# Optimization experiments

Measured on AMD Instinct MI355X. Metric: run time of the kernel, lower is better.

The kernel has to match this reference:

```python
import jax, jax.numpy as jnp
import numpy as np

CP_DIMS = (8, 8)      # control-point grid (matches init cp_dims)
EPS = 1e-10           # epsilon used by tf interpolate_spline _phi


def ndgrid(dims):
    """Normalized (y, x) grid, shape [prod(dims), 2], values in [0, 1]."""
    g = np.mgrid[:dims[0], :dims[1]].reshape(2, -1).T.astype(np.float32)
    g = g / (np.array(dims, dtype=np.float32) - 1.0)
    return jnp.asarray(g)


def _phi(r2):
    # order-2 TPS kernel on SQUARED distances: 0.5 * r2 * log(max(r2, eps))
    return 0.5 * r2 * jnp.log(jnp.maximum(r2, EPS))


def _sq_dist(a, b):
    # a: [m, d], b: [n, d] -> [m, n] squared distances
    d = a[:, None, :] - b[None, :, :]
    return jnp.sum(d * d, axis=-1)


def setup_inputs() -> dict:
    key = jax.random.key(0)
    k1, k2 = jax.random.split(key)
    vol = jax.random.normal(k1, (16, 256, 256, 16), dtype=jnp.float32)
    # small offsets in normalized [0,1] coordinates
    cp_offsets = jax.random.normal(k2, (16, 64, 2), dtype=jnp.float32) * 0.05
    return {"vol": vol, "cp_offsets": cp_offsets}


def reference(vol, cp_offsets):
    B, H, W, C = vol.shape
    cp = ndgrid(CP_DIMS)          # [n, 2] train points (fixed, inverse=False)
    q = ndgrid((H, W))            # [m, 2] query points
    n = cp.shape[0]
    m = q.shape[0]

    # ---- TPS solve (train points fixed across batch -> single LHS) ----
    A = _phi(_sq_dist(cp, cp))                              # [n, n]
    Bmat = jnp.concatenate([cp, jnp.ones((n, 1), cp.dtype)], axis=1)  # [n, 3]
    top = jnp.concatenate([A, Bmat], axis=1)                # [n, n+3]
    bot = jnp.concatenate([Bmat.T, jnp.zeros((3, 3), cp.dtype)], axis=1)
    lhs = jnp.concatenate([top, bot], axis=0)               # [n+3, n+3]

    warped = cp[None, :, :] + cp_offsets                    # [B, n, 2] train values
    rhs = jnp.concatenate([warped, jnp.zeros((B, 3, 2), vol.dtype)], axis=1)
    wv = jnp.linalg.solve(lhs[None], rhs)                   # [B, n+3, 2]
    w, v = wv[:, :n, :], wv[:, n:, :]                       # [B,n,2], [B,3,2]

    # ---- TPS apply at all pixel locations ----
    phi_q = _phi(_sq_dist(q, cp))                           # [m, n]
    q_aug = jnp.concatenate([q, jnp.ones((m, 1), q.dtype)], axis=1)  # [m, 3]
    loc = jnp.einsum('mn,bnk->bmk', phi_q, w) + jnp.einsum('mp,bpk->bmk', q_aug, v)
    # loc is (y, x) normalized; reverse -> (x, y) then scale to pixels
    x = loc[..., 1] * (W - 1)                               # [B, m]
    y = loc[..., 0] * (H - 1)

    # ---- bilinear resampling with zero padding (tf resampler semantics) ----
    x0 = jnp.floor(x); y0 = jnp.floor(y)
    wx = x - x0; wy = y - y0
    x0i = x0.astype(jnp.int32); y0i = y0.astype(jnp.int32)
    x1i = x0i + 1; y1i = y0i + 1

    vol_flat = vol.reshape(B, H * W, C)

    def gather(yi, xi):
        valid = (yi >= 0) & (yi < H) & (xi >= 0) & (xi < W)
        idx = jnp.clip(yi, 0, H - 1) * W + jnp.clip(xi, 0, W - 1)  # [B, m]
        vals = jnp.take_along_axis(vol_flat, idx[..., None], axis=1)  # [B, m, C]
        return vals * valid[..., None].astype(vol.dtype)

    out = (gather(y0i, x0i) * ((1 - wy) * (1 - wx))[..., None]
           + gather(y0i, x1i) * ((1 - wy) * wx)[..., None]
           + gather(y1i, x0i) * (wy * (1 - wx))[..., None]
           + gather(y1i, x1i) * (wy * wx)[..., None])
    return out.reshape(B, H, W, C)
```

## Files before the change

### kernel.cpp

```cpp
#include <hip/hip_runtime.h>
#include <math.h>
#include <string.h>

#define HH 256
#define WW 256
#define CC 16
#define BB 16
#define NCP 64
#define NA 67
#define WVS 68

typedef float f32x4 __attribute__((ext_vector_type(4)));

static void build_M(float* Mf , float* wv0 )
{
    static double A[NA][NA + NCP];
    for (int r = 0; r < NA; ++r) {
        for (int c = 0; c < NA; ++c) {
            double val;
            if (r < NCP && c < NCP) {
                double ry = (double)(r >> 3) / 7.0, rx = (double)(r & 7) / 7.0;
                double cy = (double)(c >> 3) / 7.0, cx = (double)(c & 7) / 7.0;
                double dy = ry - cy, dx = rx - cx;
                double r2 = dy * dy + dx * dx;
                val = 0.5 * r2 * log(r2 > 1e-10 ? r2 : 1e-10);
            } else if (r < NCP) {
                int k = c - NCP;
                val = (k == 0) ? (double)(r >> 3) / 7.0
                    : (k == 1) ? (double)(r & 7) / 7.0 : 1.0;
            } else if (c < NCP) {
                int k = r - NCP;
                val = (k == 0) ? (double)(c >> 3) / 7.0
                    : (k == 1) ? (double)(c & 7) / 7.0 : 1.0;
            } else {
                val = 0.0;
            }
            A[r][c] = val;
        }
        for (int c = 0; c < NCP; ++c) A[r][NA + c] = (r == c) ? 1.0 : 0.0;
    }
    for (int p = 0; p < NA; ++p) {
        int best = p; double bv = fabs(A[p][p]);
        for (int r = p + 1; r < NA; ++r) {
            double v = fabs(A[r][p]);
            if (v > bv) { bv = v; best = r; }
        }
        if (best != p)
            for (int j = 0; j < NA + NCP; ++j) {
                double t = A[p][j]; A[p][j] = A[best][j]; A[best][j] = t;
            }
        double ip = 1.0 / A[p][p];
        for (int j = 0; j < NA + NCP; ++j) A[p][j] *= ip;
        for (int r = 0; r < NA; ++r) {
            if (r == p) continue;
            double f = A[r][p];
            if (f != 0.0)
                for (int j = 0; j < NA + NCP; ++j) A[r][j] -= f * A[p][j];
        }
    }
    for (int r = 0; r < NA; ++r) {
        double s0 = 0.0, s1 = 0.0;
        for (int n = 0; n < NCP; ++n) {
            double m = A[r][NA + n];
            Mf[r * NCP + n] = (float)m;
            s0 += m * ((double)(n >> 3) / 7.0);
            s1 += m * ((double)(n & 7) / 7.0);
        }
        wv0[r * 2 + 0] = (float)s0;
        wv0[r * 2 + 1] = (float)s1;
    }
}

struct ConstBlob { float M[NA * NCP]; float wv0[NA * 2]; };

__global__ __launch_bounds__(256) void tps_coef_kernel(
    ConstBlob cb, const float* __restrict__ cp_offsets, float* __restrict__ wv)
{
    const int b = blockIdx.x;
    const int t = threadIdx.x;
    __shared__ float sOff[NCP * 2];
    if (t < NCP * 2) sOff[t] = cp_offsets[b * NCP * 2 + t];
    __syncthreads();
    if (t < NA * 2) {
        const int k = t & 1;
        const int r = t >> 1;
        float s = cb.wv0[r * 2 + k];
        const float* Mr = cb.M + r * NCP;
#pragma unroll
        for (int n = 0; n < NCP; ++n) s += Mr[n] * sOff[n * 2 + k];
        const float scale = (r < NCP) ? (255.0f * 0.5f * 0.69314718055994531f) : 255.0f;
        wv[(b * 2 + k) * WVS + r] = s * scale;
    } else if (t < NA * 2 + 2) {
        wv[(b * 2 + (t - NA * 2)) * WVS + 67] = 0.0f;
    }
}

__device__ __forceinline__ float quad_sum(float v)
{
    int v1 = __builtin_amdgcn_update_dpp(0, __float_as_int(v), 0xB1, 0xF, 0xF, true);
    float s = v + __int_as_float(v1);
    int v2 = __builtin_amdgcn_update_dpp(0, __float_as_int(s), 0x4E, 0xF, 0xF, true);
    return s + __int_as_float(v2);
}

__global__ __launch_bounds__(256) void tps_warp_kernel(
    const float* __restrict__ vol, const float* __restrict__ wv,
    float* __restrict__ out)
{
    const int id = blockIdx.x;
    const int xcd = id & 7;
    const int j = id >> 3;
    const int b = (xcd << 1) | (j >> 10);
    const int rr = j & 1023;
    const int y = rr >> 2;
    const int xseg = rr & 3;
    const int tid = threadIdx.x;
    const int cq = tid & 3;
    const int px = (xseg << 6) + (tid >> 2);

    const f32x4* __restrict__ w4 = (const f32x4*)(wv + (size_t)b * 2 * WVS);
    const int wo = cq << 2;
    const f32x4 wY0 = w4[wo + 0], wY1 = w4[wo + 1], wY2 = w4[wo + 2], wY3 = w4[wo + 3];
    const f32x4 wX0 = w4[17 + wo], wX1 = w4[17 + wo + 1], wX2 = w4[17 + wo + 2], wX3 = w4[17 + wo + 3];
    const f32x4 aY = w4[16];
    const f32x4 aX = w4[33];

    const float qy = (float)y * (1.0f / 255.0f);
    const float qx = (float)px * (1.0f / 255.0f);

    float dx2[8];
#pragma unroll
    for (int c = 0; c < 8; ++c) {
        float dx = qx - (float)c * (1.0f / 7.0f);
        dx2[c] = dx * dx;
    }
    const float dy0 = qy - (float)(2 * cq) * (1.0f / 7.0f);
    const float dy1 = qy - (float)(2 * cq + 1) * (1.0f / 7.0f);
    const float dy20 = dy0 * dy0, dy21 = dy1 * dy1;

    float fy = 0.f, fx = 0.f;
#pragma unroll
    for (int c = 0; c < 8; ++c) {
        float r2 = dy20 + dx2[c];
        float p = r2 * __log2f(fmaxf(r2, 1e-10f));
        float wy_ = (c < 4) ? wY0[c] : wY1[c - 4];
        float wx_ = (c < 4) ? wX0[c] : wX1[c - 4];
        fy += p * wy_;
        fx += p * wx_;
    }
#pragma unroll
    for (int c = 0; c < 8; ++c) {
        float r2 = dy21 + dx2[c];
        float p = r2 * __log2f(fmaxf(r2, 1e-10f));
        float wy_ = (c < 4) ? wY2[c] : wY3[c - 4];
        float wx_ = (c < 4) ? wX2[c] : wX3[c - 4];
        fy += p * wy_;
        fx += p * wx_;
    }
    fy = quad_sum(fy);
    fx = quad_sum(fx);
    fy += qy * aY.x + qx * aY.y + aY.z;
    fx += qy * aX.x + qx * aX.y + aX.z;

    float x0f = floorf(fx), y0f = floorf(fy);
    float wxf = fx - x0f, wyf = fy - y0f;
    int x0 = (int)x0f, y0 = (int)y0f;
    int x1 = x0 + 1, y1 = y0 + 1;
    int cx_ = (cq & 1) ? x1 : x0;
    int cy_ = (cq & 2) ? y1 : y0;
    bool valid = (cx_ >= 0) && (cx_ < WW) && (cy_ >= 0) && (cy_ < HH);
    int cxc = min(max(cx_, 0), WW - 1);
    int cyc = min(max(cy_, 0), HH - 1);
    float wc = ((cq & 1) ? wxf : 1.f - wxf) * ((cq & 2) ? wyf : 1.f - wyf)
             * (valid ? 1.f : 0.f);

    const f32x4* __restrict__ vp = (const f32x4*)vol
        + ((size_t)b * (HH * WW) + (size_t)(cyc * WW + cxc)) * (CC / 4);
    f32x4 a0 = vp[0] * wc, a1 = vp[1] * wc, a2 = vp[2] * wc, a3 = vp[3] * wc;
#pragma unroll
    for (int c = 0; c < 4; ++c) {
        a0[c] = quad_sum(a0[c]);
        a1[c] = quad_sum(a1[c]);
        a2[c] = quad_sum(a2[c]);
        a3[c] = quad_sum(a3[c]);
    }
    f32x4 o = (cq == 0) ? a0 : (cq == 1) ? a1 : (cq == 2) ? a2 : a3;

    f32x4* __restrict__ ob = (f32x4*)out
        + ((size_t)b * (HH * WW) + (size_t)y * WW) * (CC / 4);
    ob[(px << 2) + cq] = o;
}

extern "C" void kernel_launch(void* const* d_in, const int* in_sizes, int n_in,
                              void* d_out, int out_size, void* d_ws, size_t ws_size,
                              hipStream_t stream)
{
    const float* vol = (const float*)d_in[0];
    const float* cpo = (const float*)d_in[1];
    float* out = (float*)d_out;
    float* d_wv = (float*)d_ws;

    static ConstBlob cb;
    build_M(cb.M, cb.wv0);

    tps_coef_kernel<<<dim3(BB), dim3(256), 0, stream>>>(cb, cpo, d_wv);
    tps_warp_kernel<<<dim3(HH * BB * 4), dim3(256), 0, stream>>>(vol, d_wv, out);
}
```

Before: 145.5 us.

## Process full rows per block, stage gather indices/weights in LDS

Each block now covers a full 256-pixel row instead of a quarter row, looping four times over the TPS evaluation. Per-pixel corner indices and bilinear weights go to shared memory. After a barrier, each thread gathers all four corners for one 16-byte channel chunk and blends them locally, removing the DPP cross-lane reductions of the gathered data. The fmax clamp in the log term is replaced by adding a tiny epsilon to dx², which slightly changes numerics near control points. There are also four times fewer blocks and a new LDS barrier.

```diff
diff --git a/kernel.cpp b/kernel.cpp
--- a/kernel.cpp
+++ b/kernel.cpp
@@ -110,13 +110,14 @@
     const int id = blockIdx.x;
     const int xcd = id & 7;
     const int j = id >> 3;
-    const int b = (xcd << 1) | (j >> 10);
-    const int rr = j & 1023;
-    const int y = rr >> 2;
-    const int xseg = rr & 3;
+    const int b = (xcd << 1) | (j >> 8);
+    const int y = j & 255;
     const int tid = threadIdx.x;
     const int cq = tid & 3;
-    const int px = (xseg << 6) + (tid >> 2);
+    const int p0 = tid >> 2;
+
+    __shared__ int4   sI[WW];
+    __shared__ float4 sW[WW];
 
     const f32x4* __restrict__ w4 = (const f32x4*)(wv + (size_t)b * 2 * WVS);
     const int wo = cq << 2;
@@ -126,69 +127,87 @@
     const f32x4 aX = w4[33];
 
     const float qy = (float)y * (1.0f / 255.0f);
-    const float qx = (float)px * (1.0f / 255.0f);
-
-    float dx2[8];
-#pragma unroll
-    for (int c = 0; c < 8; ++c) {
-        float dx = qx - (float)c * (1.0f / 7.0f);
-        dx2[c] = dx * dx;
-    }
     const float dy0 = qy - (float)(2 * cq) * (1.0f / 7.0f);
     const float dy1 = qy - (float)(2 * cq + 1) * (1.0f / 7.0f);
     const float dy20 = dy0 * dy0, dy21 = dy1 * dy1;
 
-    float fy = 0.f, fx = 0.f;
-#pragma unroll
-    for (int c = 0; c < 8; ++c) {
-        float r2 = dy20 + dx2[c];
-        float p = r2 * __log2f(fmaxf(r2, 1e-10f));
-        float wy_ = (c < 4) ? wY0[c] : wY1[c - 4];
-        float wx_ = (c < 4) ? wX0[c] : wX1[c - 4];
-        fy += p * wy_;
-        fx += p * wx_;
-    }
-#pragma unroll
-    for (int c = 0; c < 8; ++c) {
-        float r2 = dy21 + dx2[c];
-        float p = r2 * __log2f(fmaxf(r2, 1e-10f));
-        float wy_ = (c < 4) ? wY2[c] : wY3[c - 4];
-        float wx_ = (c < 4) ? wX2[c] : wX3[c - 4];
-        fy += p * wy_;
-        fx += p * wx_;
-    }
-    fy = quad_sum(fy);
-    fx = quad_sum(fx);
-    fy += qy * aY.x + qx * aY.y + aY.z;
-    fx += qy * aX.x + qx * aX.y + aX.z;
-
-    float x0f = floorf(fx), y0f = floorf(fy);
-    float wxf = fx - x0f, wyf = fy - y0f;
-    int x0 = (int)x0f, y0 = (int)y0f;
-    int x1 = x0 + 1, y1 = y0 + 1;
-    int cx_ = (cq & 1) ? x1 : x0;
-    int cy_ = (cq & 2) ? y1 : y0;
-    bool valid = (cx_ >= 0) && (cx_ < WW) && (cy_ >= 0) && (cy_ < HH);
-    int cxc = min(max(cx_, 0), WW - 1);
-    int cyc = min(max(cy_, 0), HH - 1);
-    float wc = ((cq & 1) ? wxf : 1.f - wxf) * ((cq & 2) ? wyf : 1.f - wyf)
-             * (valid ? 1.f : 0.f);
-
-    const f32x4* __restrict__ vp = (const f32x4*)vol
-        + ((size_t)b * (HH * WW) + (size_t)(cyc * WW + cxc)) * (CC / 4);
-    f32x4 a0 = vp[0] * wc, a1 = vp[1] * wc, a2 = vp[2] * wc, a3 = vp[3] * wc;
-#pragma unroll
-    for (int c = 0; c < 4; ++c) {
-        a0[c] = quad_sum(a0[c]);
-        a1[c] = quad_sum(a1[c]);
-        a2[c] = quad_sum(a2[c]);
-        a3[c] = quad_sum(a3[c]);
-    }
-    f32x4 o = (cq == 0) ? a0 : (cq == 1) ? a1 : (cq == 2) ? a2 : a3;
-
-    f32x4* __restrict__ ob = (f32x4*)out
-        + ((size_t)b * (HH * WW) + (size_t)y * WW) * (CC / 4);
-    ob[(px << 2) + cq] = o;
+#pragma unroll
+    for (int g = 0; g < 4; ++g) {
+        const int px = (g << 6) + p0;
+        const float qx = (float)px * (1.0f / 255.0f);
+
+        float dx2[8];
+#pragma unroll
+        for (int c = 0; c < 8; ++c) {
+            float dx = qx - (float)c * (1.0f / 7.0f);
+            dx2[c] = dx * dx + 1e-12f;
+        }
+        float fy = 0.f, fx = 0.f;
+#pragma unroll
+        for (int c = 0; c < 8; ++c) {
+            float r2 = dy20 + dx2[c];
+            float p = r2 * __log2f(r2);
+            float wy_ = (c < 4) ? wY0[c] : wY1[c - 4];
+            float wx_ = (c < 4) ? wX0[c] : wX1[c - 4];
+            fy += p * wy_;
+            fx += p * wx_;
+        }
+#pragma unroll
+        for (int c = 0; c < 8; ++c) {
+            float r2 = dy21 + dx2[c];
+            float p = r2 * __log2f(r2);
+            float wy_ = (c < 4) ? wY2[c] : wY3[c - 4];
+            float wx_ = (c < 4) ? wX2[c] : wX3[c - 4];
+            fy += p * wy_;
+            fx += p * wx_;
+        }
+        fy = quad_sum(fy);
+        fx = quad_sum(fx);
+        fy += qy * aY.x + qx * aY.y + aY.z;
+        fx += qy * aX.x + qx * aX.y + aX.z;
+
+        float x0f = floorf(fx), y0f = floorf(fy);
+        float wxf = fx - x0f, wyf = fy - y0f;
+        int x0 = (int)x0f, y0 = (int)y0f;
+        int x1 = x0 + 1, y1 = y0 + 1;
+        bool vx0 = (x0 >= 0) && (x0 < WW), vx1 = (x1 >= 0) && (x1 < WW);
+        bool vy0 = (y0 >= 0) && (y0 < HH), vy1 = (y1 >= 0) && (y1 < HH);
+        int x0c = min(max(x0, 0), WW - 1), x1c = min(max(x1, 0), WW - 1);
+        int y0c = min(max(y0, 0), HH - 1), y1c = min(max(y1, 0), HH - 1);
+        if (cq == 0) {
+            sI[px] = make_int4((y0c * WW + x0c) * 4, (y0c * WW + x1c) * 4,
+                               (y1c * WW + x0c) * 4, (y1c * WW + x1c) * 4);
+        } else if (cq == 1) {
+            float4 w4v;
+            w4v.x = (1.f - wyf) * (1.f - wxf) * ((vy0 && vx0) ? 1.f : 0.f);
+            w4v.y = (1.f - wyf) * wxf         * ((vy0 && vx1) ? 1.f : 0.f);
+            w4v.z = wyf * (1.f - wxf)         * ((vy1 && vx0) ? 1.f : 0.f);
+            w4v.w = wyf * wxf                 * ((vy1 && vx1) ? 1.f : 0.f);
+            sW[px] = w4v;
+        }
+    }
+    __syncthreads();
+
+    const float4* __restrict__ vb =
+        (const float4*)vol + (size_t)b * (HH * WW * (CC / 4));
+    float4* __restrict__ ob =
+        (float4*)out + ((size_t)b * HH * WW + (size_t)y * WW) * (CC / 4);
+#pragma unroll
+    for (int k = 0; k < 4; ++k) {
+        const int p = p0 + 64 * k;
+        int4   I = sI[p];
+        float4 Wt = sW[p];
+        float4 a  = vb[I.x + cq];
+        float4 bq = vb[I.y + cq];
+        float4 c_ = vb[I.z + cq];
+        float4 d_ = vb[I.w + cq];
+        float4 r;
+        r.x = a.x * Wt.x + bq.x * Wt.y + c_.x * Wt.z + d_.x * Wt.w;
+        r.y = a.y * Wt.x + bq.y * Wt.y + c_.y * Wt.z + d_.y * Wt.w;
+        r.z = a.z * Wt.x + bq.z * Wt.y + c_.z * Wt.z + d_.z * Wt.w;
+        r.w = a.w * Wt.x + bq.w * Wt.y + c_.w * Wt.z + d_.w * Wt.w;
+        ob[tid + 256 * k] = r;
+    }
 }
 
 extern "C" void kernel_launch(void* const* d_in, const int* in_sizes, int n_in,
@@ -204,5 +223,5 @@
     build_M(cb.M, cb.wv0);
 
     tps_coef_kernel<<<dim3(BB), dim3(256), 0, stream>>>(cb, cpo, d_wv);
-    tps_warp_kernel<<<dim3(HH * BB * 4), dim3(256), 0, stream>>>(vol, d_wv, out);
-}
+    tps_warp_kernel<<<dim3(HH * BB), dim3(256), 0, stream>>>(vol, d_wv, out);
+}
```

After: 137.0 us. 5.8% less time.
